# Kernel tuning notes

Hardware: AMD Instinct MI355X
Metric: run time of the kernel (lower is better)

The kernel has to match this reference:

```python
import jax, jax.numpy as jnp
import numpy as np

H, W = 80, 80
LOWPASS = 0.3   # 3DGS low-pass filter added to 2D covariance diagonal
NEAR = 0.2      # near-plane cull depth


def quat_to_rot(q):
    # q: [N,4] (w,x,y,z) -> [N,3,3]
    w, x, y, z = q[..., 0], q[..., 1], q[..., 2], q[..., 3]
    return jnp.stack([
        jnp.stack([1 - 2 * (y * y + z * z), 2 * (x * y - w * z), 2 * (x * z + w * y)], -1),
        jnp.stack([2 * (x * y + w * z), 1 - 2 * (x * x + z * z), 2 * (y * z - w * x)], -1),
        jnp.stack([2 * (x * z - w * y), 2 * (y * z + w * x), 1 - 2 * (x * x + y * y)], -1),
    ], -2)


def setup_inputs() -> dict:
    key = jax.random.key(0)
    k1, k2 = jax.random.split(key)
    vsize = 1.25
    def mids(lo, hi, lim):
        g = np.arange(lo, hi + 1e-6, vsize)
        return ((g[:-1] + g[1:]) / 2.0)[:lim]
    xy = mids(-20.0, 20.0, 200)   # 32 midpoints
    zz = mids(-4.0, 4.0, 16)      # 6 midpoints
    X, Y, Z = np.meshgrid(xy, xy, zz, indexing='ij')
    pc_xyz = jnp.asarray(np.stack([X, Y, Z], -1).reshape(-1, 3), jnp.float32)  # [6144,3]
    N = pc_xyz.shape[0]
    B, NC, C = 1, 6, 32
    vox_features = jax.random.normal(k1, (B, N, C), jnp.float32)
    density = jax.random.normal(k2, (B, N), jnp.float32)
    scales = jnp.full((N, 1), float(np.log(vsize)), jnp.float32)
    rots = jnp.concatenate([jnp.ones((N, 1)), jnp.zeros((N, 3))], -1).astype(jnp.float32)
    # 6 surround cameras at origin, yaw = k*60deg; cam axes: x=right, y=up-ish, z=forward
    yaws = np.arange(NC) * (2 * np.pi / NC)
    f = np.stack([np.cos(yaws), np.sin(yaws), np.zeros(NC)], -1)
    r = np.stack([np.sin(yaws), -np.cos(yaws), np.zeros(NC)], -1)
    u = np.cross(f, r)
    Rw2c = np.stack([r, u, f], 1)  # rows are camera axes -> world2cam rotation [NC,3,3]
    cam_rot = jnp.asarray(Rw2c[None], jnp.float32)          # [B,NC,3,3]
    cam_trans = jnp.zeros((B, NC, 3), jnp.float32)          # [B,NC,3]
    cam_intr = jnp.asarray(np.tile(np.array([45.0, 45.0, W / 2.0, H / 2.0], np.float32), (B, NC, 1)))
    return dict(vox_features=vox_features, density=density, cam_rot=cam_rot,
                cam_trans=cam_trans, cam_intr=cam_intr, pc_xyz=pc_xyz,
                scales=scales, rots=rots)


def _render_one(Rcw, t, intr, pc_xyz, Mcov, opacity, feats):
    # Rcw [3,3], t [3], intr [4]; Mcov [N,3,3] = R*diag(s); opacity [N]; feats [N,C]
    fx, fy, cx, cy = intr[0], intr[1], intr[2], intr[3]
    cam = pc_xyz @ Rcw.T + t                    # [N,3] camera-frame means
    tz = jnp.maximum(cam[:, 2], 1e-6)
    valid = (cam[:, 2] > NEAR).astype(pc_xyz.dtype)
    u = fx * cam[:, 0] / tz + cx
    v = fy * cam[:, 1] / tz + cy
    z0 = jnp.zeros_like(tz)
    J = jnp.stack([jnp.stack([fx / tz, z0, -fx * cam[:, 0] / tz ** 2], -1),
                   jnp.stack([z0, fy / tz, -fy * cam[:, 1] / tz ** 2], -1)], -2)  # [N,2,3]
    A = jnp.einsum('nij,jk->nik', J, Rcw)       # J @ W  [N,2,3]
    Bm = jnp.einsum('nij,njk->nik', A, Mcov)    # [N,2,3]
    cov = jnp.einsum('nij,nkj->nik', Bm, Bm)    # 2D covariance [N,2,2]
    a = cov[:, 0, 0] + LOWPASS
    b = cov[:, 0, 1]
    c = cov[:, 1, 1] + LOWPASS
    det = a * c - b * b
    ia, ib, ic = c / det, -b / det, a / det
    # depth-sort (invalid gaussians pushed to the back)
    order = jnp.argsort(tz + (1.0 - valid) * 1e6)
    u, v, ia, ib, ic = u[order], v[order], ia[order], ib[order], ic[order]
    op_s, feat_s, valid_s = opacity[order], feats[order], valid[order]
    px = jnp.arange(W, dtype=pc_xyz.dtype)
    py = jnp.arange(H, dtype=pc_xyz.dtype)
    dx = px[None, None, :] - u[:, None, None]   # [N,1,W] -> broadcast [N,H,W]
    dy = py[None, :, None] - v[:, None, None]   # [N,H,1]
    power = (-0.5 * (ia[:, None, None] * dx * dx + ic[:, None, None] * dy * dy)
             - ib[:, None, None] * dx * dy)
    g = jnp.exp(jnp.minimum(power, 0.0))
    alpha = jnp.clip(op_s[:, None, None] * g, 0.0, 0.99) * valid_s[:, None, None]
    Tcum = jnp.cumprod(1.0 - alpha, axis=0)
    Texc = jnp.concatenate([jnp.ones((1, H, W), alpha.dtype), Tcum[:-1]], 0)  # exclusive transmittance
    return jnp.einsum('nhw,nc->chw', Texc * alpha, feat_s)


def reference(vox_features, density, cam_rot, cam_trans, cam_intr, pc_xyz, scales, rots):
    Bsz, N, C = vox_features.shape
    Rg = quat_to_rot(rots)                      # [N,3,3]
    s = jnp.exp(scales)                         # [N,1] isotropic scale
    Mcov = Rg * s[:, :, None]                   # R @ diag(s,s,s)
    outs = []
    for b in range(Bsz):
        op = jax.nn.softplus(density[b]).reshape(-1)        # opacity activation
        feats = vox_features[b].reshape(-1, C)
        def rone(args):
            R_, t_, K_ = args
            return _render_one(R_, t_, K_, pc_xyz, Mcov, op, feats)
        out_b = jax.lax.map(rone, (cam_rot[b], cam_trans[b], cam_intr[b]))  # [NC,C,H,W]
        outs.append(out_b)
    return jnp.stack(outs)                      # [B,NC,C,H,W]
```

## Files before the change

### kernel.cpp

```cpp
#include <hip/hip_runtime.h>

#define NEARV    0.2f
#define LOWPASSV 0.3f

constexpr int HH = 80, WW = 80;
constexpr int CFE = 32;
constexpr int NZ = 6;

constexpr int NCELL = 1024;
constexpr int HMAX = NCELL * NZ;

typedef unsigned long long u64;
typedef unsigned int u32;
typedef float v2f __attribute__((ext_vector_type(2)));

__global__ __launch_bounds__(256) void prep_kernel(
    const float* __restrict__ pc_xyz, const float* __restrict__ cam_rot,
    const float* __restrict__ cam_trans, const float* __restrict__ cam_intr,
    const float* __restrict__ density, const float* __restrict__ scales,
    int N, int NC,
    int* __restrict__ counts, float4* __restrict__ hdrA,
    float4* __restrict__ hdrB)
{
  __shared__ u32 sk[NCELL];
  __shared__ int rnk[64];
  __shared__ u32 wred[4];

  const int cam = blockIdx.y;
  const int tid = threadIdx.x;
  const float* R = cam_rot + cam*9;
  const float* t = cam_trans + cam*3;
  const float R20 = R[6], R21 = R[7], R22 = R[8];
  const float t2  = t[2];

  int vcnt = 0;
  #pragma unroll
  for (int e4 = 0; e4 < NCELL/256; ++e4) {
    const int cell = e4*256 + tid;
    const int i0 = cell * NZ;
    u32 key22 = 0x3FFFFFu;
    if (i0 < N) {
      float c2 = R20*pc_xyz[i0*3+0] + R21*pc_xyz[i0*3+1] + R22*pc_xyz[i0*3+2] + t2;
      if (c2 > NEARV) {
        u32 b = __float_as_uint(c2) - 0x3E000000u;
        b = b < 0x03FFFF00u ? b : 0x03FFFF00u;
        key22 = b >> 4;
        ++vcnt;
      }
    }
    sk[cell] = (key22 << 10) | (u32)cell;
  }
  __syncthreads();

  const int cbase = blockIdx.x * 64;
  const int cl = tid >> 2;
  const int q  = tid & 3;
  const u32 mykey = sk[cbase + cl];
  const uint4* k4 = (const uint4*)sk;
  int r = 0;
  #pragma unroll 8
  for (int i = 0; i < 64; ++i) {
    const uint4 kv = k4[q*64 + i];
    r += (int)(kv.x < mykey) + (int)(kv.y < mykey)
       + (int)(kv.z < mykey) + (int)(kv.w < mykey);
  }
  r += __shfl_xor(r, 1, 64);
  r += __shfl_xor(r, 2, 64);
  if (q == 0) rnk[cl] = r;

  if (blockIdx.x == 0) {
    #pragma unroll
    for (int off = 32; off > 0; off >>= 1) vcnt += __shfl_down(vcnt, off, 64);
    if ((tid & 63) == 0) wred[tid >> 6] = (u32)vcnt;
  }
  __syncthreads();
  if (blockIdx.x == 0 && tid == 0)
    counts[cam] = (int)(wred[0] + wred[1] + wred[2] + wred[3]) * NZ;

  const float* intr = cam_intr + cam*4;
  const float fx = intr[0], fy = intr[1], cx = intr[2], cy = intr[3];
  const float R0=R[0],R1=R[1],R2=R[2],R3=R[3],R4=R[4],R5=R[5];
  const float t0=t[0],t1=t[1];
  const int b = cam / NC;
  float4* hA = hdrA + (size_t)cam * HMAX;
  float4* hB = hdrB + (size_t)cam * HMAX;

  for (int g = tid; g < 64*NZ; g += 256) {
    const int cl2 = g / NZ, iz = g - cl2*NZ;
    const int n  = (cbase + cl2) * NZ + iz;
    const int kq = rnk[cl2] * NZ + iz;
    if (n >= N) continue;

    const float p0 = pc_xyz[n*3+0], p1 = pc_xyz[n*3+1], p2 = pc_xyz[n*3+2];
    const float c0 = R0*p0 + R1*p1 + R2*p2 + t0;
    const float c1 = R3*p0 + R4*p1 + R5*p2 + t1;
    const float c2 = R20*p0 + R21*p1 + R22*p2 + t2;
    const float tz = fmaxf(c2, 1e-6f);
    const float itz = 1.0f / tz;
    const float u = fx*c0*itz + cx;
    const float v = fy*c1*itz + cy;
    const float j00 = fx*itz, j02 = -(fx*c0*itz)*itz;
    const float j11 = fy*itz, j12 = -(fy*c1*itz)*itz;
    const float s = expf(scales[n]);
    const float s2 = s*s;
    const float cov00 = s2*(j00*j00 + j02*j02);
    const float cov01 = s2*(j02*j12);
    const float cov11 = s2*(j11*j11 + j12*j12);
    const float a = cov00 + LOWPASSV, bb = cov01, cc = cov11 + LOWPASSV;
    const float det = a*cc - bb*bb;
    const float idet = 1.0f / det;
    const float mid = 0.5f*(a + cc);
    const float dd = sqrtf(fmaxf(mid*mid - det, 0.f));
    float r2 = 32.f * (mid + dd);
    const float dens = density[(size_t)b*N + n];
    const float op = fmaxf(dens, 0.f) + log1pf(expf(-fabsf(dens)));
    const float sx = fminf(fmaxf(u, 0.f), (float)(WW-1)) - u;
    const float sy = fminf(fmaxf(v, 0.f), (float)(HH-1)) - v;
    if (sx*sx + sy*sy > r2) r2 = -1.0f;

    const float L = 1.4426950408889634f;
    const float A2 = -0.5f * (cc*idet) * L;
    const float C2 = -0.5f * (a*idet)  * L;
    const float B2 =         (bb*idet) * L;

    hA[kq] = make_float4(u, v, A2, B2);
    hB[kq] = make_float4(C2, op, r2, __int_as_float(n));
  }
}

__global__ __launch_bounds__(64) void render_kernel(
    const float* __restrict__ vox,
    const float4* __restrict__ hdrA, const float4* __restrict__ hdrB,
    const int* __restrict__ counts,
    float* __restrict__ out, int N, int NC)
{
  __shared__ int   cgi[64];
  __shared__ float4 sfeat[64];

  const int cam = blockIdx.y;
  const int tile = blockIdx.x;
  const int tx = tile % (WW/16), ty = tile / (WW/16);
  const int lane = threadIdx.x;
  const int lx = lane & 15, ly = lane >> 4;
  const int px = tx*16 + lx, py = ty*4 + ly;
  const float fpx = (float)px, fpy = (float)py;
  const float tx0 = (float)(tx*16), tx1 = tx0 + 15.f;
  const float ty0 = (float)(ty*4),  ty1 = ty0 + 3.f;
  const int count = counts[cam];
  const int b = cam / NC;
  const float4* hA = hdrA + (size_t)cam * HMAX;
  const float4* hB = hdrB + (size_t)cam * HMAX;
  const float4* voxb = (const float4*)vox + (size_t)b * N * (CFE/4);

  v2f acc2[CFE/2];
  #pragma unroll
  for (int i = 0; i < CFE/2; ++i) { acc2[i].x = 0.f; acc2[i].y = 0.f; }
  float T = 1.0f;
  bool done = false;

#define RDLN(x, l) __uint_as_float(__builtin_amdgcn_readlane(__float_as_uint(x), (l)))

#define LOAD4(Aarr, Barr, base_) do {                                   \
    _Pragma("unroll")                                                   \
    for (int d_ = 0; d_ < 4; ++d_) {                                    \
      const int kn_ = min((base_) + d_*64 + lane, count - 1);           \
      Aarr[d_] = hA[kn_]; Barr[d_] = hB[kn_];                           \
    } } while (0)

#define PROCESS_CHUNK(k0_, a0_, b0_) do {                               \
    const int ki = (k0_) + lane;                                        \
       \
    const float gu = (a0_).x, gv = (a0_).y;                             \
    const float gA = (a0_).z, gB = (a0_).w, gC = (b0_).x;               \
    const float dxl = tx0 - gu, dxh = tx1 - gu;                         \
    const float dyl = ty0 - gv, dyh = ty1 - gv;                         \
    const float X = fmaxf(dxl, fminf(0.f, dxh));                        \
    const float Y = fmaxf(dyl, fminf(0.f, dyh));                        \
    const float dyv = fmaxf(dyl, fminf((gB*X) / (-2.0f*gC), dyh));      \
    const float P1 = gA*X*X + gC*dyv*dyv + gB*X*dyv;                    \
    const float dxv = fmaxf(dxl, fminf((gB*Y) / (-2.0f*gA), dxh));      \
    const float P2 = gA*dxv*dxv + gC*Y*Y + gB*dxv*Y;                    \
    const bool hit = (ki < count) && (fmaxf(P1, P2) > -23.0831f);       \
    const u64 m = __ballot(hit);                                        \
    const int P = __popcll(m);                                          \
    if (P == 0) continue;                                               \
    if (hit) {                                                          \
      const int pos = (int)__popcll(m & ((1ull << lane) - 1ull));       \
      cgi[pos] = __float_as_int((b0_).w);                               \
    }                                                                   \
    __builtin_amdgcn_wave_barrier();   \
    const int sl = lane >> 3, sc = lane & 7;                            \
    float4 pf = voxb[(size_t)cgi[min(sl, P - 1)] * (CFE/4) + sc];       \
    u64 mm_ = m;                       \
    for (int j = 0; j < P; j += 8) {                                    \
      float al[8];                                                      \
      _Pragma("unroll")                                                 \
      for (int qq = 0; qq < 8; ++qq) {                                  \
        const int idx = j + qq;                                         \
        int lq = 0;                                                     \
        if (mm_) { lq = (int)__builtin_ctzll(mm_); mm_ &= mm_ - 1; }    \
        const float su  = RDLN((a0_).x, lq);                            \
        const float sv  = RDLN((a0_).y, lq);                            \
        const float sA2 = RDLN((a0_).z, lq);                            \
        const float sB2 = RDLN((a0_).w, lq);                            \
        const float sC2 = RDLN((b0_).x, lq);                            \
        const float sop = RDLN((b0_).y, lq);                            \
        const float dx = fpx - su, dy = fpy - sv;                       \
        const float pl2 = sA2*(dx*dx) + sC2*(dy*dy) + sB2*(dx*dy);      \
        float av = fminf(sop * __builtin_exp2f(fminf(pl2, 0.f)), 0.99f); \
        av = (pl2 > -23.0831f) ? av : 0.f;       \
        al[qq] = (idx < P) ? av : 0.f;                                  \
      }                                                                 \
      sfeat[lane] = pf;                            \
      if (j + 8 < P) {                            \
        const int si = min(j + 8 + sl, P - 1);                          \
        pf = voxb[(size_t)cgi[si] * (CFE/4) + sc];                      \
      }                                                                 \
      __builtin_amdgcn_wave_barrier();   \
      _Pragma("unroll")                                                 \
      for (int qq = 0; qq < 8; ++qq) {                                  \
        const float w = T * al[qq];                                     \
        T -= w;                                                         \
        if (__any(w > 1e-8f)) {                                         \
          const float4* fj = &sfeat[qq * 8];                            \
          v2f w2; w2.x = w; w2.y = w;                                   \
          _Pragma("unroll")                                             \
          for (int c8 = 0; c8 < CFE/4; ++c8) {                          \
            const float4 fv = fj[c8];                                   \
            v2f lo; lo.x = fv.x; lo.y = fv.y;                           \
            v2f hi; hi.x = fv.z; hi.y = fv.w;                           \
            asm("v_pk_fma_f32 %0, %1, %2, %0"                           \
                : "+v"(acc2[c8*2+0]) : "v"(w2), "v"(lo));               \
            asm("v_pk_fma_f32 %0, %1, %2, %0"                           \
                : "+v"(acc2[c8*2+1]) : "v"(w2), "v"(hi));               \
          }                                                             \
        }                                                               \
      }                                                                 \
      if (__all(T < 1e-3f)) { done = true; break; }                     \
      __builtin_amdgcn_wave_barrier();  \
    }                                                                   \
  } while (0)

  if (count > 0) {
    float4 A0x[4], B0x[4], A1x[4], B1x[4];
    const int nquad = (count + 255) >> 8;
    LOAD4(A0x, B0x, 0);

    for (int q = 0; q < nquad && !done; q += 2) {
      if (q + 1 < nquad) LOAD4(A1x, B1x, (q+1)*256);
      #pragma unroll
      for (int d = 0; d < 4; ++d) {
        if (done) break;
        const int k0 = q*256 + d*64;
        if (k0 >= count) break;
        PROCESS_CHUNK(k0, A0x[d], B0x[d]);
      }
      if (done || q + 1 >= nquad) break;
      if (q + 2 < nquad) LOAD4(A0x, B0x, (q+2)*256);
      #pragma unroll
      for (int d = 0; d < 4; ++d) {
        if (done) break;
        const int k0 = (q+1)*256 + d*64;
        if (k0 >= count) break;
        PROCESS_CHUNK(k0, A1x[d], B1x[d]);
      }
    }
  }
#undef PROCESS_CHUNK
#undef LOAD4
#undef RDLN

  float* ob = out + (((size_t)cam * CFE) * HH + py) * WW + px;
  #pragma unroll
  for (int c8 = 0; c8 < CFE/2; ++c8) {
    ob[(size_t)(2*c8+0) * HH * WW] = acc2[c8].x;
    ob[(size_t)(2*c8+1) * HH * WW] = acc2[c8].y;
  }
}

extern "C" void kernel_launch(void* const* d_in, const int* in_sizes, int n_in,
                              void* d_out, int out_size, void* d_ws, size_t ws_size,
                              hipStream_t stream) {
  const float* vox       = (const float*)d_in[0];
  const float* density   = (const float*)d_in[1];
  const float* cam_rot   = (const float*)d_in[2];
  const float* cam_trans = (const float*)d_in[3];
  const float* cam_intr  = (const float*)d_in[4];
  const float* pc_xyz    = (const float*)d_in[5];
  const float* scales    = (const float*)d_in[6];
  float* out = (float*)d_out;

  const int N    = in_sizes[5] / 3;
  const int NCAM = in_sizes[4] / 4;
  const int B    = in_sizes[1] / N;
  const int NC   = NCAM / B;

  unsigned char* ws = (unsigned char*)d_ws;
  int* countsPtr = (int*)ws;
  float4* hdrA   = (float4*)(ws + 32768);
  float4* hdrB   = (float4*)(ws + 32768 + (size_t)NCAM * HMAX * sizeof(float4));

  prep_kernel<<<dim3(NCELL/64, NCAM), 256, 0, stream>>>(
      pc_xyz, cam_rot, cam_trans, cam_intr, density, scales, N, NC,
      countsPtr, hdrA, hdrB);
  render_kernel<<<dim3((WW/16)*(HH/4), NCAM), 64, 0, stream>>>(
      vox, hdrA, hdrB, countsPtr, out, N, NC);
}
```

Measured before the change: 79.68 us.

## Split each tile's depth-sorted gaussian list across two waves and merge

Each render block now runs two waves. Each wave composites one half of the sorted gaussian list for the same 16x4 pixel tile, and the second half's accumulated colour is merged as front + T_front * back through shared memory. The goal is to shorten the serial per-tile compositing chain and double the parallelism available, which helps with only 6 cameras x 100 tiles. The cost is that the back wave may do work that the front wave's early termination would have skipped. A shared flag tries to stop it early, and there is extra shared memory and block-level synchronisation.

```diff
diff --git a/kernel.cpp b/kernel.cpp
--- a/kernel.cpp
+++ b/kernel.cpp
@@ -128,19 +128,23 @@
   }
 }
 
-__global__ __launch_bounds__(64) void render_kernel(
+__global__ __launch_bounds__(128) void render_kernel(
     const float* __restrict__ vox,
     const float4* __restrict__ hdrA, const float4* __restrict__ hdrB,
     const int* __restrict__ counts,
     float* __restrict__ out, int N, int NC)
 {
-  __shared__ int   cgi[64];
-  __shared__ float4 sfeat[64];
+  __shared__ int    cgi[2][64];
+  __shared__ float4 sfeat[2][64];
+  __shared__ v2f    segC[64][CFE/2 + 1];
+  __shared__ int    sflag;
 
   const int cam = blockIdx.y;
   const int tile = blockIdx.x;
   const int tx = tile % (WW/16), ty = tile / (WW/16);
-  const int lane = threadIdx.x;
+  const int tidb = threadIdx.x;
+  const int wv = tidb >> 6;
+  const int lane = tidb & 63;
   const int lx = lane & 15, ly = lane >> 4;
   const int px = tx*16 + lx, py = ty*4 + ly;
   const float fpx = (float)px, fpy = (float)py;
@@ -152,6 +156,17 @@
   const float4* hB = hdrB + (size_t)cam * HMAX;
   const float4* voxb = (const float4*)vox + (size_t)b * N * (CFE/4);
 
+  int half = ((count/2 + 63) >> 6) << 6;
+  if (half > count) half = count;
+  const int kb = wv ? half : 0;
+  const int ke = wv ? count : half;
+
+  if (tidb == 0) sflag = 0;
+  __syncthreads();
+
+  int* cgw = cgi[wv];
+  float4* sfw = sfeat[wv];
+
   v2f acc2[CFE/2];
   #pragma unroll
   for (int i = 0; i < CFE/2; ++i) { acc2[i].x = 0.f; acc2[i].y = 0.f; }
@@ -163,7 +178,7 @@
 #define LOAD4(Aarr, Barr, base_) do {                                   \
     _Pragma("unroll")                                                   \
     for (int d_ = 0; d_ < 4; ++d_) {                                    \
-      const int kn_ = min((base_) + d_*64 + lane, count - 1);           \
+      const int kn_ = min((base_) + d_*64 + lane, ke - 1);              \
       Aarr[d_] = hA[kn_]; Barr[d_] = hB[kn_];                           \
     } } while (0)
 
@@ -180,17 +195,17 @@
     const float P1 = gA*X*X + gC*dyv*dyv + gB*X*dyv;                    \
     const float dxv = fmaxf(dxl, fminf((gB*Y) / (-2.0f*gA), dxh));      \
     const float P2 = gA*dxv*dxv + gC*Y*Y + gB*dxv*Y;                    \
-    const bool hit = (ki < count) && (fmaxf(P1, P2) > -23.0831f);       \
+    const bool hit = (ki < ke) && (fmaxf(P1, P2) > -23.0831f);          \
     const u64 m = __ballot(hit);                                        \
     const int P = __popcll(m);                                          \
     if (P == 0) continue;                                               \
     if (hit) {                                                          \
       const int pos = (int)__popcll(m & ((1ull << lane) - 1ull));       \
-      cgi[pos] = __float_as_int((b0_).w);                               \
+      cgw[pos] = __float_as_int((b0_).w);                               \
     }                                                                   \
     __builtin_amdgcn_wave_barrier();   \
     const int sl = lane >> 3, sc = lane & 7;                            \
-    float4 pf = voxb[(size_t)cgi[min(sl, P - 1)] * (CFE/4) + sc];       \
+    float4 pf = voxb[(size_t)cgw[min(sl, P - 1)] * (CFE/4) + sc];       \
     u64 mm_ = m;                       \
     for (int j = 0; j < P; j += 8) {                                    \
       float al[8];                                                      \
@@ -211,10 +226,10 @@
         av = (pl2 > -23.0831f) ? av : 0.f;       \
         al[qq] = (idx < P) ? av : 0.f;                                  \
       }                                                                 \
-      sfeat[lane] = pf;                            \
+      sfw[lane] = pf;                              \
       if (j + 8 < P) {                            \
         const int si = min(j + 8 + sl, P - 1);                          \
-        pf = voxb[(size_t)cgi[si] * (CFE/4) + sc];                      \
+        pf = voxb[(size_t)cgw[si] * (CFE/4) + sc];                      \
       }                                                                 \
       __builtin_amdgcn_wave_barrier();   \
       _Pragma("unroll")                                                 \
@@ -222,7 +237,7 @@
         const float w = T * al[qq];                                     \
         T -= w;                                                         \
         if (__any(w > 1e-8f)) {                                         \
-          const float4* fj = &sfeat[qq * 8];                            \
+          const float4* fj = &sfw[qq * 8];                              \
           v2f w2; w2.x = w; w2.y = w;                                   \
           _Pragma("unroll")                                             \
           for (int c8 = 0; c8 < CFE/4; ++c8) {                          \
@@ -241,27 +256,29 @@
     }                                                                   \
   } while (0)
 
-  if (count > 0) {
+  if (ke > kb) {
     float4 A0x[4], B0x[4], A1x[4], B1x[4];
-    const int nquad = (count + 255) >> 8;
-    LOAD4(A0x, B0x, 0);
+    const int nquad = (ke - kb + 255) >> 8;
+    LOAD4(A0x, B0x, kb);
 
     for (int q = 0; q < nquad && !done; q += 2) {
-      if (q + 1 < nquad) LOAD4(A1x, B1x, (q+1)*256);
+      if (q + 1 < nquad) LOAD4(A1x, B1x, kb + (q+1)*256);
       #pragma unroll
       for (int d = 0; d < 4; ++d) {
         if (done) break;
-        const int k0 = q*256 + d*64;
-        if (k0 >= count) break;
+        if (wv && *(volatile int*)&sflag) { done = true; break; }
+        const int k0 = kb + q*256 + d*64;
+        if (k0 >= ke) break;
         PROCESS_CHUNK(k0, A0x[d], B0x[d]);
       }
       if (done || q + 1 >= nquad) break;
-      if (q + 2 < nquad) LOAD4(A0x, B0x, (q+2)*256);
+      if (q + 2 < nquad) LOAD4(A0x, B0x, kb + (q+2)*256);
       #pragma unroll
       for (int d = 0; d < 4; ++d) {
         if (done) break;
-        const int k0 = (q+1)*256 + d*64;
-        if (k0 >= count) break;
+        if (wv && *(volatile int*)&sflag) { done = true; break; }
+        const int k0 = kb + (q+1)*256 + d*64;
+        if (k0 >= ke) break;
         PROCESS_CHUNK(k0, A1x[d], B1x[d]);
       }
     }
@@ -270,11 +287,28 @@
 #undef LOAD4
 #undef RDLN
 
-  float* ob = out + (((size_t)cam * CFE) * HH + py) * WW + px;
-  #pragma unroll
-  for (int c8 = 0; c8 < CFE/2; ++c8) {
-    ob[(size_t)(2*c8+0) * HH * WW] = acc2[c8].x;
-    ob[(size_t)(2*c8+1) * HH * WW] = acc2[c8].y;
+  if (wv == 0 && done) *(volatile int*)&sflag = 1;
+
+  __syncthreads();
+  if (wv == 1) {
+    #pragma unroll
+    for (int c8 = 0; c8 < CFE/2; ++c8) segC[lane][c8] = acc2[c8];
+  }
+  __syncthreads();
+  if (wv == 0) {
+    v2f t2v; t2v.x = T; t2v.y = T;
+    #pragma unroll
+    for (int c8 = 0; c8 < CFE/2; ++c8) {
+      const v2f c1 = segC[lane][c8];
+      acc2[c8].x = fmaf(t2v.x, c1.x, acc2[c8].x);
+      acc2[c8].y = fmaf(t2v.y, c1.y, acc2[c8].y);
+    }
+    float* ob = out + (((size_t)cam * CFE) * HH + py) * WW + px;
+    #pragma unroll
+    for (int c8 = 0; c8 < CFE/2; ++c8) {
+      ob[(size_t)(2*c8+0) * HH * WW] = acc2[c8].x;
+      ob[(size_t)(2*c8+1) * HH * WW] = acc2[c8].y;
+    }
   }
 }
 
@@ -303,6 +337,6 @@
   prep_kernel<<<dim3(NCELL/64, NCAM), 256, 0, stream>>>(
       pc_xyz, cam_rot, cam_trans, cam_intr, density, scales, N, NC,
       countsPtr, hdrA, hdrB);
-  render_kernel<<<dim3((WW/16)*(HH/4), NCAM), 64, 0, stream>>>(
+  render_kernel<<<dim3((WW/16)*(HH/4), NCAM), 128, 0, stream>>>(
       vox, hdrA, hdrB, countsPtr, out, N, NC);
 }
```

New measurement: 92.29 us. +15.8%, slower.
